# Kernel tuning notes

Hardware: AMD Instinct MI355X
Metric: run time of the kernel (lower is better)

Reference implementation:

```python
import jax, jax.numpy as jnp
import numpy as np

B, T, H = 8192, 256, 128


def setup_inputs() -> dict:
    key = jax.random.key(0)
    ks = jax.random.split(key, 12)
    s = 1.0 / np.sqrt(H)
    inp = {
        "x_seq": jax.random.normal(ks[0], (B, T), dtype=jnp.float32),
        "m_seq": (jax.random.uniform(ks[1], (B, T)) < 0.5).astype(jnp.float32),
        # W_c: Linear(hidden, 1)
        "Wc_w": jax.random.uniform(ks[2], (1, H), minval=-s, maxval=s),
        "Wc_b": jax.random.uniform(ks[3], (1,), minval=-s, maxval=s),
        # W_x: Linear(1, hidden)
        "Wx_w": jax.random.uniform(ks[4], (H, 1), minval=-1.0, maxval=1.0),
        "Wx_b": jax.random.uniform(ks[5], (H,), minval=-1.0, maxval=1.0),
        # GRUCell(hidden+1, hidden): gates ordered (r, z, n) as in torch
        "W_ih": jax.random.uniform(ks[6], (3 * H, H + 1), minval=-s, maxval=s),
        "W_hh": jax.random.uniform(ks[7], (3 * H, H), minval=-s, maxval=s),
        "b_ih": jax.random.uniform(ks[8], (3 * H,), minval=-s, maxval=s),
        "b_hh": jax.random.uniform(ks[9], (3 * H,), minval=-s, maxval=s),
        # out: Linear(hidden, 1)
        "out_w": jax.random.uniform(ks[10], (1, H), minval=-s, maxval=s),
        "out_b": jax.random.uniform(ks[11], (1,), minval=-s, maxval=s),
    }
    return inp


def reference(x_seq, m_seq, Wc_w, Wc_b, Wx_w, Wx_b, W_ih, W_hh, b_ih, b_hh, out_w, out_b):
    Bd, Td = x_seq.shape
    Hd = W_hh.shape[1]

    def step(h, xs):
        x_t, m_t = xs  # each [B]
        # c_t = tanh(W_c h)[:, 0]
        c_t = jnp.tanh(h @ Wc_w.T + Wc_b)[:, 0]  # [B]
        x_imp = m_t * x_t + (1.0 - m_t) * c_t  # [B]
        # feat = relu(W_x x_imp): Linear(1, H) on scalar input
        feat = jax.nn.relu(x_imp[:, None] * Wx_w[:, 0][None, :] + Wx_b)  # [B, H]
        inp = jnp.concatenate([feat, m_t[:, None]], axis=1)  # [B, H+1]
        # torch GRUCell math, gate order (r, z, n)
        gi = inp @ W_ih.T + b_ih  # [B, 3H]
        gh = h @ W_hh.T + b_hh  # [B, 3H]
        i_r, i_z, i_n = gi[:, :Hd], gi[:, Hd:2 * Hd], gi[:, 2 * Hd:]
        h_r, h_z, h_n = gh[:, :Hd], gh[:, Hd:2 * Hd], gh[:, 2 * Hd:]
        r = jax.nn.sigmoid(i_r + h_r)
        z = jax.nn.sigmoid(i_z + h_z)
        n = jnp.tanh(i_n + r * h_n)
        h_new = (1.0 - z) * n + z * h
        pred = (h_new @ out_w.T + out_b)[:, 0]  # [B]
        return h_new, (pred, c_t)

    h0 = jnp.zeros((Bd, Hd), dtype=x_seq.dtype)
    xs = (x_seq.T, m_seq.T)  # [T, B]
    _, (preds, comps) = jax.lax.scan(step, h0, xs)
    return preds.T, comps.T  # each [B, T]
```

## Files before the change

kernel.cpp:

```cpp
#include <hip/hip_runtime.h>

#define B_ 8192
#define T_ 256
#define H_ 128
#define ROWS 32
#define NTH 512

typedef __attribute__((ext_vector_type(4))) float f32x4;
typedef __attribute__((ext_vector_type(4))) short short4_t;
typedef __attribute__((ext_vector_type(8))) short short8_t;
typedef __attribute__((ext_vector_type(8))) _Float16 half8;
typedef __attribute__((ext_vector_type(2))) _Float16 half2_t;
typedef __attribute__((ext_vector_type(4))) unsigned int uint4_t;

__device__ __forceinline__ float fast_exp(float x) {
    return __builtin_amdgcn_exp2f(x * 1.4426950408889634f);
}
__device__ __forceinline__ float sigm(float x) {
    return __builtin_amdgcn_rcpf(1.0f + fast_exp(-x));
}
__device__ __forceinline__ float tanh_f(float x) {
    return 1.0f - 2.0f * __builtin_amdgcn_rcpf(1.0f + fast_exp(2.0f * x));
}
__device__ __forceinline__ short h16bits(float v) {
    return __builtin_bit_cast(short, (_Float16)v);
}
__device__ __forceinline__ float h16f(short s) {
    return (float)__builtin_bit_cast(_Float16, s);
}
__device__ __forceinline__ float red16(float v) {
    v += __builtin_bit_cast(float, __builtin_amdgcn_update_dpp(0, __builtin_bit_cast(int, v), 0x111, 0xf, 0xf, true));
    v += __builtin_bit_cast(float, __builtin_amdgcn_update_dpp(0, __builtin_bit_cast(int, v), 0x112, 0xf, 0xf, true));
    v += __builtin_bit_cast(float, __builtin_amdgcn_update_dpp(0, __builtin_bit_cast(int, v), 0x114, 0xf, 0xf, true));
    v += __builtin_bit_cast(float, __builtin_amdgcn_update_dpp(0, __builtin_bit_cast(int, v), 0x118, 0xf, 0xf, true));
    return v;
}

__global__ __launch_bounds__(NTH, 2) void brits_kernel(
    const float* __restrict__ x_seq, const float* __restrict__ m_seq,
    const float* __restrict__ Wc_w,  const float* __restrict__ Wc_b,
    const float* __restrict__ Wx_w,  const float* __restrict__ Wx_b,
    const float* __restrict__ W_ih,  const float* __restrict__ W_hh,
    const float* __restrict__ b_ih,  const float* __restrict__ b_hh,
    const float* __restrict__ out_w, const float* __restrict__ out_b,
    float* __restrict__ out)
{
    __shared__ __align__(16) short feat_s[2][4][512];
    __shared__ __align__(16) short h_s[2][2][4][512];
    __shared__ __align__(16) short x_all[T_][ROWS];
    __shared__ __align__(16) short m_all[T_][ROWS];
    __shared__ __align__(16) short comp_sh[ROWS][264];
    __shared__ __align__(16) short pred_sh[ROWS][264];
    __shared__ __align__(16) float part_c[ROWS][8];
    __shared__ __align__(16) float wx_s[H_];
    __shared__ __align__(16) float bx_s[H_];
    __shared__ __align__(16) short ow_s[4][512];

    const int tid  = threadIdx.x;
    const int lane = tid & 63;
    const int wv   = tid >> 6;
    const int kg   = lane >> 4;
    const int ln16 = lane & 15;
    const int rb   = kg * 4;
    const long b0  = (long)blockIdx.x * ROWS;

    const int rowA = tid & 31;
    const int qA   = tid >> 5;

    const float cb = Wc_b[0];
    const float ob = out_b[0];

    const int cH = wv * 16 + ln16;
    const int cR = cH, cZ = cH + 128, cN = cH + 256;
    const float bR  = b_ih[cR] + b_hh[cR];
    const float bZ  = b_ih[cZ] + b_hh[cZ];
    const float bNi = b_ih[cN];
    const float bNh = b_hh[cN];
    const float WmR = W_ih[cR * 129 + 128];
    const float WmZ = W_ih[cZ * 129 + 128];
    const float WmN = W_ih[cN * 129 + 128];
    const float wcc = Wc_w[cH];

    half8 wr[8], wz[8], wn[8];
#pragma unroll
    for (int kc = 0; kc < 8; ++kc) {
        const float *pr, *pz, *pn;
        if (kc < 4) {
            const int off = kc * 32 + kg * 8;
            pr = W_ih + cR * 129 + off;
            pz = W_ih + cZ * 129 + off;
            pn = W_ih + cN * 129 + off;
        } else {
            const int off = (kc - 4) * 32 + kg * 8;
            pr = W_hh + cR * 128 + off;
            pz = W_hh + cZ * 128 + off;
            pn = W_hh + cN * 128 + off;
        }
#pragma unroll
        for (int e = 0; e < 8; ++e) {
            wr[kc][e] = (_Float16)pr[e];
            wz[kc][e] = (_Float16)pz[e];
            wn[kc][e] = (_Float16)pn[e];
        }
    }

    {
        const int prow = tid >> 4;
        const int ptb  = (tid & 15) * 16;
        const float* xp = x_seq + (b0 + prow) * T_ + ptb;
        const float* mp = m_seq + (b0 + prow) * T_ + ptb;
#pragma unroll
        for (int i = 0; i < 4; ++i) {
            f32x4 xv = *(const f32x4*)(xp + 4 * i);
            f32x4 mv = *(const f32x4*)(mp + 4 * i);
#pragma unroll
            for (int j = 0; j < 4; ++j) {
                x_all[ptb + 4 * i + j][prow] = h16bits(xv[j]);
                m_all[ptb + 4 * i + j][prow] = h16bits(mv[j]);
            }
        }
    }
    if (tid < H_) { wx_s[tid] = Wx_w[tid]; bx_s[tid] = Wx_b[tid]; }
    {
        short8_t z8 = {0, 0, 0, 0, 0, 0, 0, 0};
        *(short8_t*)((short*)h_s + tid * 8) = z8;
    }
    if (tid < 256) ((float*)part_c)[tid] = 0.0f;
#pragma unroll
    for (int i = 0; i < 4; ++i) {
        const int idx = tid * 4 + i;
        const int c = idx >> 9, rl = idx & 511;
        const int ln = rl >> 3, j = rl & 7;
        const int col = ln & 15;
        const int k = 32 * c + (ln >> 4) * 8 + j;
        ((short*)ow_s)[idx] = (col == 0) ? h16bits(out_w[k]) : (short)0;
    }

    f32x4 h0reg = {0.f, 0.f, 0.f, 0.f};
    f32x4 h1reg = {0.f, 0.f, 0.f, 0.f};
    __syncthreads();

    for (int t = 0; t < T_; ++t) {
        const int pb = t & 1, nb = pb ^ 1;

        f32x4 p0 = *(const f32x4*)&part_c[rowA][0];
        f32x4 p1 = *(const f32x4*)&part_c[rowA][4];
        const float sc = ((p0[0] + p0[1]) + (p0[2] + p0[3])) +
                         ((p1[0] + p1[1]) + (p1[2] + p1[3]));
        const float c_t = tanh_f(sc + cb);
        const float xv = h16f(x_all[t][rowA]);
        const float mv = h16f(m_all[t][rowA]);
        const float xi = (mv != 0.0f) ? xv : c_t;
        if (qA == 0) comp_sh[rowA][t] = h16bits(c_t);
        {
            f32x4 wxa = *(const f32x4*)&wx_s[qA * 8];
            f32x4 wxb = *(const f32x4*)&wx_s[qA * 8 + 4];
            f32x4 bxa = *(const f32x4*)&bx_s[qA * 8];
            f32x4 bxb = *(const f32x4*)&bx_s[qA * 8 + 4];
            f32x4 fa, fb;
#pragma unroll
            for (int j = 0; j < 4; ++j) {
                fa[j] = fmaxf(xi * wxa[j] + bxa[j], 0.0f);
                fb[j] = fmaxf(xi * wxb[j] + bxb[j], 0.0f);
            }
            uint4_t pk;
            pk[0] = __builtin_bit_cast(unsigned int, __builtin_amdgcn_cvt_pkrtz(fa[0], fa[1]));
            pk[1] = __builtin_bit_cast(unsigned int, __builtin_amdgcn_cvt_pkrtz(fa[2], fa[3]));
            pk[2] = __builtin_bit_cast(unsigned int, __builtin_amdgcn_cvt_pkrtz(fb[0], fb[1]));
            pk[3] = __builtin_bit_cast(unsigned int, __builtin_amdgcn_cvt_pkrtz(fb[2], fb[3]));
            *(uint4_t*)&feat_s[rowA >> 4][qA >> 2][((rowA & 15) + 16 * (qA & 3)) * 8] = pk;
        }

        short4_t m4a = *(const short4_t*)&m_all[t][rb];
        short4_t m4b = *(const short4_t*)&m_all[t][16 + rb];
        f32x4 aR0, aZ0, aNi0, aNh0, aR1, aZ1, aNi1, aNh1;
#pragma unroll
        for (int e = 0; e < 4; ++e) {
            const float m0 = h16f(m4a[e]), m1 = h16f(m4b[e]);
            aR0[e]  = bR  + m0 * WmR;  aR1[e]  = bR  + m1 * WmR;
            aZ0[e]  = bZ  + m0 * WmZ;  aZ1[e]  = bZ  + m1 * WmZ;
            aNi0[e] = bNi + m0 * WmN;  aNi1[e] = bNi + m1 * WmN;
            aNh0[e] = bNh;             aNh1[e] = bNh;
        }
        f32x4 pacc = {0.f, 0.f, 0.f, 0.f};
        __syncthreads();

#pragma unroll
        for (int kc = 0; kc < 4; ++kc) {
            half8 a0 = __builtin_bit_cast(half8, *(const short8_t*)&feat_s[0][kc][lane * 8]);
            half8 a1 = __builtin_bit_cast(half8, *(const short8_t*)&feat_s[1][kc][lane * 8]);
            aR0  = __builtin_amdgcn_mfma_f32_16x16x32_f16(a0, wr[kc], aR0, 0, 0, 0);
            aZ0  = __builtin_amdgcn_mfma_f32_16x16x32_f16(a0, wz[kc], aZ0, 0, 0, 0);
            aNi0 = __builtin_amdgcn_mfma_f32_16x16x32_f16(a0, wn[kc], aNi0, 0, 0, 0);
            aR1  = __builtin_amdgcn_mfma_f32_16x16x32_f16(a1, wr[kc], aR1, 0, 0, 0);
            aZ1  = __builtin_amdgcn_mfma_f32_16x16x32_f16(a1, wz[kc], aZ1, 0, 0, 0);
            aNi1 = __builtin_amdgcn_mfma_f32_16x16x32_f16(a1, wn[kc], aNi1, 0, 0, 0);
        }
#pragma unroll
        for (int kc = 0; kc < 4; ++kc) {
            half8 a0 = __builtin_bit_cast(half8, *(const short8_t*)&h_s[pb][0][kc][lane * 8]);
            half8 a1 = __builtin_bit_cast(half8, *(const short8_t*)&h_s[pb][1][kc][lane * 8]);
            aR0  = __builtin_amdgcn_mfma_f32_16x16x32_f16(a0, wr[4 + kc], aR0, 0, 0, 0);
            aZ0  = __builtin_amdgcn_mfma_f32_16x16x32_f16(a0, wz[4 + kc], aZ0, 0, 0, 0);
            aNh0 = __builtin_amdgcn_mfma_f32_16x16x32_f16(a0, wn[4 + kc], aNh0, 0, 0, 0);
            aR1  = __builtin_amdgcn_mfma_f32_16x16x32_f16(a1, wr[4 + kc], aR1, 0, 0, 0);
            aZ1  = __builtin_amdgcn_mfma_f32_16x16x32_f16(a1, wz[4 + kc], aZ1, 0, 0, 0);
            aNh1 = __builtin_amdgcn_mfma_f32_16x16x32_f16(a1, wn[4 + kc], aNh1, 0, 0, 0);
            if (wv == 4) {
                half8 bfr = __builtin_bit_cast(half8, *(const short8_t*)&ow_s[kc][lane * 8]);
                pacc = __builtin_amdgcn_mfma_f32_16x16x32_f16(a0, bfr, pacc, 0, 0, 0);
            }
            if (wv == 5) {
                half8 bfr = __builtin_bit_cast(half8, *(const short8_t*)&ow_s[kc][lane * 8]);
                pacc = __builtin_amdgcn_mfma_f32_16x16x32_f16(a1, bfr, pacc, 0, 0, 0);
            }
        }

        f32x4 hn0, hn1;
#pragma unroll
        for (int e = 0; e < 4; ++e) {
            const float r0 = sigm(aR0[e]), z0 = sigm(aZ0[e]);
            const float n0 = tanh_f(aNi0[e] + r0 * aNh0[e]);
            hn0[e] = z0 * (h0reg[e] - n0) + n0;
            const float r1 = sigm(aR1[e]), z1 = sigm(aZ1[e]);
            const float n1 = tanh_f(aNi1[e] + r1 * aNh1[e]);
            hn1[e] = z1 * (h1reg[e] - n1) + n1;
        }
        h0reg = hn0; h1reg = hn1;

        const int hc = cH >> 5;
        const int hbase = ((cH & 31) >> 3) * 128 + (cH & 7);
#pragma unroll
        for (int e = 0; e < 4; ++e) {
            h_s[nb][0][hc][hbase + (rb + e) * 8] = h16bits(hn0[e]);
            h_s[nb][1][hc][hbase + (rb + e) * 8] = h16bits(hn1[e]);
        }
#pragma unroll
        for (int e = 0; e < 4; ++e) {
            const float s0 = red16(hn0[e] * wcc);
            const float s1 = red16(hn1[e] * wcc);
            if (ln16 == 15) {
                part_c[rb + e][wv]      = s0;
                part_c[16 + rb + e][wv] = s1;
            }
        }
        if ((wv == 4 || wv == 5) && ln16 == 0 && t > 0) {
#pragma unroll
            for (int e = 0; e < 4; ++e)
                pred_sh[(wv - 4) * 16 + rb + e][t - 1] = h16bits(pacc[e] + ob);
        }
        __syncthreads();
    }

    if (wv == 4 || wv == 5) {
        f32x4 pacc = {0.f, 0.f, 0.f, 0.f};
#pragma unroll
        for (int kc = 0; kc < 4; ++kc) {
            half8 a = __builtin_bit_cast(half8, *(const short8_t*)&h_s[0][wv - 4][kc][lane * 8]);
            half8 bfr = __builtin_bit_cast(half8, *(const short8_t*)&ow_s[kc][lane * 8]);
            pacc = __builtin_amdgcn_mfma_f32_16x16x32_f16(a, bfr, pacc, 0, 0, 0);
        }
        if (ln16 == 0) {
#pragma unroll
            for (int e = 0; e < 4; ++e)
                pred_sh[(wv - 4) * 16 + rb + e][T_ - 1] = h16bits(pacc[e] + ob);
        }
    }
    __syncthreads();

    {
        const int orow = tid >> 4;
        const int oc   = (tid & 15) * 16;
        short8_t r0 = *(const short8_t*)&pred_sh[orow][oc];
        short8_t r1 = *(const short8_t*)&pred_sh[orow][oc + 8];
        float* gp = out + (b0 + orow) * T_ + oc;
#pragma unroll
        for (int i = 0; i < 4; ++i) {
            f32x4 o;
            o[0] = h16f((i < 2) ? r0[i * 4 + 0] : r1[(i - 2) * 4 + 0]);
            o[1] = h16f((i < 2) ? r0[i * 4 + 1] : r1[(i - 2) * 4 + 1]);
            o[2] = h16f((i < 2) ? r0[i * 4 + 2] : r1[(i - 2) * 4 + 2]);
            o[3] = h16f((i < 2) ? r0[i * 4 + 3] : r1[(i - 2) * 4 + 3]);
            *(f32x4*)(gp + 4 * i) = o;
        }
        short8_t c0v = *(const short8_t*)&comp_sh[orow][oc];
        short8_t c1v = *(const short8_t*)&comp_sh[orow][oc + 8];
        float* gc = out + (long)B_ * T_ + (b0 + orow) * T_ + oc;
#pragma unroll
        for (int i = 0; i < 4; ++i) {
            f32x4 o;
            o[0] = h16f((i < 2) ? c0v[i * 4 + 0] : c1v[(i - 2) * 4 + 0]);
            o[1] = h16f((i < 2) ? c0v[i * 4 + 1] : c1v[(i - 2) * 4 + 1]);
            o[2] = h16f((i < 2) ? c0v[i * 4 + 2] : c1v[(i - 2) * 4 + 2]);
            o[3] = h16f((i < 2) ? c0v[i * 4 + 3] : c1v[(i - 2) * 4 + 3]);
            *(f32x4*)(gc + 4 * i) = o;
        }
    }
}

extern "C" void kernel_launch(void* const* d_in, const int* in_sizes, int n_in,
                              void* d_out, int out_size, void* d_ws, size_t ws_size,
                              hipStream_t stream) {
    const float* x_seq = (const float*)d_in[0];
    const float* m_seq = (const float*)d_in[1];
    const float* Wc_w  = (const float*)d_in[2];
    const float* Wc_b  = (const float*)d_in[3];
    const float* Wx_w  = (const float*)d_in[4];
    const float* Wx_b  = (const float*)d_in[5];
    const float* W_ih  = (const float*)d_in[6];
    const float* W_hh  = (const float*)d_in[7];
    const float* b_ih  = (const float*)d_in[8];
    const float* b_hh  = (const float*)d_in[9];
    const float* out_w = (const float*)d_in[10];
    const float* out_b = (const float*)d_in[11];
    float* out = (float*)d_out;

    dim3 grid(B_ / ROWS);
    dim3 block(NTH);
    brits_kernel<<<grid, block, 0, stream>>>(x_seq, m_seq, Wc_w, Wc_b, Wx_w, Wx_b,
                                             W_ih, W_hh, b_ih, b_hh, out_w, out_b, out);
}
```

Before: 636.2 us.

## Halve rows per block, pack h in fp16, fuse pred into reduction

Rows per block drop from 32 to 16 and launch bounds rise from 2 to 4 blocks per SM, trading fewer MFMAs per block for more resident blocks and more grid parallelism. The output projection is no longer a separate MFMA on two waves. It now runs as a packed fp16 DPP reduction alongside the Wc reduction, so one half2 reduce gives both c_t and pred. Hidden state and the bias/mask terms are kept in packed fp16, which cuts registers but lowers accumulation precision in the reductions.

```diff
diff --git a/kernel.cpp b/kernel.cpp
--- a/kernel.cpp
+++ b/kernel.cpp
@@ -3,7 +3,7 @@
 #define B_ 8192
 #define T_ 256
 #define H_ 128
-#define ROWS 32
+#define ROWS 16
 #define NTH 512
 
 typedef __attribute__((ext_vector_type(4))) float f32x4;
@@ -11,6 +11,7 @@
 typedef __attribute__((ext_vector_type(8))) short short8_t;
 typedef __attribute__((ext_vector_type(8))) _Float16 half8;
 typedef __attribute__((ext_vector_type(2))) _Float16 half2_t;
+typedef __attribute__((ext_vector_type(2))) unsigned int uint2_t;
 typedef __attribute__((ext_vector_type(4))) unsigned int uint4_t;
 
 __device__ __forceinline__ float fast_exp(float x) {
@@ -28,15 +29,24 @@
 __device__ __forceinline__ float h16f(short s) {
     return (float)__builtin_bit_cast(_Float16, s);
 }
-__device__ __forceinline__ float red16(float v) {
-    v += __builtin_bit_cast(float, __builtin_amdgcn_update_dpp(0, __builtin_bit_cast(int, v), 0x111, 0xf, 0xf, true));
-    v += __builtin_bit_cast(float, __builtin_amdgcn_update_dpp(0, __builtin_bit_cast(int, v), 0x112, 0xf, 0xf, true));
-    v += __builtin_bit_cast(float, __builtin_amdgcn_update_dpp(0, __builtin_bit_cast(int, v), 0x114, 0xf, 0xf, true));
-    v += __builtin_bit_cast(float, __builtin_amdgcn_update_dpp(0, __builtin_bit_cast(int, v), 0x118, 0xf, 0xf, true));
+__device__ __forceinline__ unsigned pk2(float lo, float hi) {
+    return __builtin_bit_cast(unsigned, __builtin_amdgcn_cvt_pkrtz(lo, hi));
+}
+__device__ __forceinline__ half2_t h2(unsigned u) {
+    return __builtin_bit_cast(half2_t, u);
+}
+__device__ __forceinline__ unsigned pkadd(unsigned a, unsigned b) {
+    return __builtin_bit_cast(unsigned, (half2_t)(h2(a) + h2(b)));
+}
+__device__ __forceinline__ unsigned red16_pk(unsigned v) {
+    v = pkadd(v, (unsigned)__builtin_amdgcn_update_dpp(0, (int)v, 0x111, 0xf, 0xf, true));
+    v = pkadd(v, (unsigned)__builtin_amdgcn_update_dpp(0, (int)v, 0x112, 0xf, 0xf, true));
+    v = pkadd(v, (unsigned)__builtin_amdgcn_update_dpp(0, (int)v, 0x114, 0xf, 0xf, true));
+    v = pkadd(v, (unsigned)__builtin_amdgcn_update_dpp(0, (int)v, 0x118, 0xf, 0xf, true));
     return v;
 }
 
-__global__ __launch_bounds__(NTH, 2) void brits_kernel(
+__global__ __launch_bounds__(NTH, 4) void brits_kernel(
     const float* __restrict__ x_seq, const float* __restrict__ m_seq,
     const float* __restrict__ Wc_w,  const float* __restrict__ Wc_b,
     const float* __restrict__ Wx_w,  const float* __restrict__ Wx_b,
@@ -45,16 +55,15 @@
     const float* __restrict__ out_w, const float* __restrict__ out_b,
     float* __restrict__ out)
 {
-    __shared__ __align__(16) short feat_s[2][4][512];
-    __shared__ __align__(16) short h_s[2][2][4][512];
+    __shared__ __align__(16) short feat_s[4][512];
+    __shared__ __align__(16) short h_s[2][4][512];
     __shared__ __align__(16) short x_all[T_][ROWS];
     __shared__ __align__(16) short m_all[T_][ROWS];
     __shared__ __align__(16) short comp_sh[ROWS][264];
     __shared__ __align__(16) short pred_sh[ROWS][264];
-    __shared__ __align__(16) float part_c[ROWS][8];
+    __shared__ __align__(16) unsigned part_cp[ROWS][8];
     __shared__ __align__(16) float wx_s[H_];
     __shared__ __align__(16) float bx_s[H_];
-    __shared__ __align__(16) short ow_s[4][512];
 
     const int tid  = threadIdx.x;
     const int lane = tid & 63;
@@ -64,22 +73,21 @@
     const int rb   = kg * 4;
     const long b0  = (long)blockIdx.x * ROWS;
 
-    const int rowA = tid & 31;
-    const int qA   = tid >> 5;
+    const int rowA = tid & 15;
+    const int kqA  = tid >> 4;
 
     const float cb = Wc_b[0];
     const float ob = out_b[0];
 
     const int cH = wv * 16 + ln16;
     const int cR = cH, cZ = cH + 128, cN = cH + 256;
-    const float bR  = b_ih[cR] + b_hh[cR];
-    const float bZ  = b_ih[cZ] + b_hh[cZ];
-    const float bNi = b_ih[cN];
-    const float bNh = b_hh[cN];
-    const float WmR = W_ih[cR * 129 + 128];
-    const float WmZ = W_ih[cZ * 129 + 128];
-    const float WmN = W_ih[cN * 129 + 128];
+
+    const unsigned bRZ  = pk2(b_ih[cR] + b_hh[cR], b_ih[cZ] + b_hh[cZ]);
+    const unsigned WmRZ = pk2(W_ih[cR * 129 + 128], W_ih[cZ * 129 + 128]);
+    const unsigned bNN  = pk2(b_ih[cN], b_hh[cN]);
+    const unsigned WmN0 = pk2(W_ih[cN * 129 + 128], 0.0f);
     const float wcc = Wc_w[cH];
+    const float owc = out_w[cH];
 
     half8 wr[8], wz[8], wn[8];
 #pragma unroll
@@ -105,18 +113,18 @@
     }
 
     {
-        const int prow = tid >> 4;
-        const int ptb  = (tid & 15) * 16;
-        const float* xp = x_seq + (b0 + prow) * T_ + ptb;
-        const float* mp = m_seq + (b0 + prow) * T_ + ptb;
-#pragma unroll
-        for (int i = 0; i < 4; ++i) {
+        const int prow = tid >> 5;
+        const int pc0  = (tid & 31) * 8;
+        const float* xp = x_seq + (b0 + prow) * T_ + pc0;
+        const float* mp = m_seq + (b0 + prow) * T_ + pc0;
+#pragma unroll
+        for (int i = 0; i < 2; ++i) {
             f32x4 xv = *(const f32x4*)(xp + 4 * i);
             f32x4 mv = *(const f32x4*)(mp + 4 * i);
 #pragma unroll
             for (int j = 0; j < 4; ++j) {
-                x_all[ptb + 4 * i + j][prow] = h16bits(xv[j]);
-                m_all[ptb + 4 * i + j][prow] = h16bits(mv[j]);
+                x_all[pc0 + 4 * i + j][prow] = h16bits(xv[j]);
+                m_all[pc0 + 4 * i + j][prow] = h16bits(mv[j]);
             }
         }
     }
@@ -125,174 +133,127 @@
         short8_t z8 = {0, 0, 0, 0, 0, 0, 0, 0};
         *(short8_t*)((short*)h_s + tid * 8) = z8;
     }
-    if (tid < 256) ((float*)part_c)[tid] = 0.0f;
-#pragma unroll
-    for (int i = 0; i < 4; ++i) {
-        const int idx = tid * 4 + i;
-        const int c = idx >> 9, rl = idx & 511;
-        const int ln = rl >> 3, j = rl & 7;
-        const int col = ln & 15;
-        const int k = 32 * c + (ln >> 4) * 8 + j;
-        ((short*)ow_s)[idx] = (col == 0) ? h16bits(out_w[k]) : (short)0;
-    }
-
-    f32x4 h0reg = {0.f, 0.f, 0.f, 0.f};
-    f32x4 h1reg = {0.f, 0.f, 0.f, 0.f};
+    if (tid < ROWS * 8) ((unsigned*)part_cp)[tid] = 0u;
+
+    unsigned hp0 = 0u, hp1 = 0u;
     __syncthreads();
 
     for (int t = 0; t < T_; ++t) {
         const int pb = t & 1, nb = pb ^ 1;
 
-        f32x4 p0 = *(const f32x4*)&part_c[rowA][0];
-        f32x4 p1 = *(const f32x4*)&part_c[rowA][4];
-        const float sc = ((p0[0] + p0[1]) + (p0[2] + p0[3])) +
-                         ((p1[0] + p1[1]) + (p1[2] + p1[3]));
-        const float c_t = tanh_f(sc + cb);
+        uint4_t u0 = *(const uint4_t*)&part_cp[rowA][0];
+        uint4_t u1 = *(const uint4_t*)&part_cp[rowA][4];
+        unsigned sacc = pkadd(pkadd(pkadd(u0[0], u0[1]), pkadd(u0[2], u0[3])),
+                              pkadd(pkadd(u1[0], u1[1]), pkadd(u1[2], u1[3])));
+        const half2_t sv = h2(sacc);
+        const float c_t = tanh_f((float)sv[0] + cb);
+        if (kqA == 0) comp_sh[rowA][t] = h16bits(c_t);
+        if (kqA == 1 && t > 0) pred_sh[rowA][t - 1] = h16bits((float)sv[1] + ob);
+
         const float xv = h16f(x_all[t][rowA]);
         const float mv = h16f(m_all[t][rowA]);
         const float xi = (mv != 0.0f) ? xv : c_t;
-        if (qA == 0) comp_sh[rowA][t] = h16bits(c_t);
         {
-            f32x4 wxa = *(const f32x4*)&wx_s[qA * 8];
-            f32x4 wxb = *(const f32x4*)&wx_s[qA * 8 + 4];
-            f32x4 bxa = *(const f32x4*)&bx_s[qA * 8];
-            f32x4 bxb = *(const f32x4*)&bx_s[qA * 8 + 4];
-            f32x4 fa, fb;
-#pragma unroll
-            for (int j = 0; j < 4; ++j) {
-                fa[j] = fmaxf(xi * wxa[j] + bxa[j], 0.0f);
-                fb[j] = fmaxf(xi * wxb[j] + bxb[j], 0.0f);
-            }
-            uint4_t pk;
-            pk[0] = __builtin_bit_cast(unsigned int, __builtin_amdgcn_cvt_pkrtz(fa[0], fa[1]));
-            pk[1] = __builtin_bit_cast(unsigned int, __builtin_amdgcn_cvt_pkrtz(fa[2], fa[3]));
-            pk[2] = __builtin_bit_cast(unsigned int, __builtin_amdgcn_cvt_pkrtz(fb[0], fb[1]));
-            pk[3] = __builtin_bit_cast(unsigned int, __builtin_amdgcn_cvt_pkrtz(fb[2], fb[3]));
-            *(uint4_t*)&feat_s[rowA >> 4][qA >> 2][((rowA & 15) + 16 * (qA & 3)) * 8] = pk;
-        }
-
-        short4_t m4a = *(const short4_t*)&m_all[t][rb];
-        short4_t m4b = *(const short4_t*)&m_all[t][16 + rb];
-        f32x4 aR0, aZ0, aNi0, aNh0, aR1, aZ1, aNi1, aNh1;
+            const int k = kqA * 4;
+            f32x4 wx4 = *(const f32x4*)&wx_s[k];
+            f32x4 bx4 = *(const f32x4*)&bx_s[k];
+            float f0 = fmaxf(xi * wx4[0] + bx4[0], 0.0f);
+            float f1 = fmaxf(xi * wx4[1] + bx4[1], 0.0f);
+            float f2 = fmaxf(xi * wx4[2] + bx4[2], 0.0f);
+            float f3 = fmaxf(xi * wx4[3] + bx4[3], 0.0f);
+            uint2_t pk; pk[0] = pk2(f0, f1); pk[1] = pk2(f2, f3);
+            const int o = (kqA >> 1) & 3, j = (kqA & 1) * 4;
+            *(uint2_t*)&feat_s[kqA >> 3][(rowA + 16 * o) * 8 + j] = pk;
+        }
+
+        short4_t m4 = *(const short4_t*)&m_all[t][rb];
+        f32x4 aR, aZ, aNi, aNh;
 #pragma unroll
         for (int e = 0; e < 4; ++e) {
-            const float m0 = h16f(m4a[e]), m1 = h16f(m4b[e]);
-            aR0[e]  = bR  + m0 * WmR;  aR1[e]  = bR  + m1 * WmR;
-            aZ0[e]  = bZ  + m0 * WmZ;  aZ1[e]  = bZ  + m1 * WmZ;
-            aNi0[e] = bNi + m0 * WmN;  aNi1[e] = bNi + m1 * WmN;
-            aNh0[e] = bNh;             aNh1[e] = bNh;
-        }
-        f32x4 pacc = {0.f, 0.f, 0.f, 0.f};
+            unsigned mu = (unsigned)(unsigned short)m4[e];
+            mu |= mu << 16;
+            half2_t rz = h2(mu) * h2(WmRZ) + h2(bRZ);
+            half2_t nn = h2(mu) * h2(WmN0) + h2(bNN);
+            aR[e] = (float)rz[0]; aZ[e] = (float)rz[1];
+            aNi[e] = (float)nn[0]; aNh[e] = (float)nn[1];
+        }
         __syncthreads();
 
 #pragma unroll
         for (int kc = 0; kc < 4; ++kc) {
-            half8 a0 = __builtin_bit_cast(half8, *(const short8_t*)&feat_s[0][kc][lane * 8]);
-            half8 a1 = __builtin_bit_cast(half8, *(const short8_t*)&feat_s[1][kc][lane * 8]);
-            aR0  = __builtin_amdgcn_mfma_f32_16x16x32_f16(a0, wr[kc], aR0, 0, 0, 0);
-            aZ0  = __builtin_amdgcn_mfma_f32_16x16x32_f16(a0, wz[kc], aZ0, 0, 0, 0);
-            aNi0 = __builtin_amdgcn_mfma_f32_16x16x32_f16(a0, wn[kc], aNi0, 0, 0, 0);
-            aR1  = __builtin_amdgcn_mfma_f32_16x16x32_f16(a1, wr[kc], aR1, 0, 0, 0);
-            aZ1  = __builtin_amdgcn_mfma_f32_16x16x32_f16(a1, wz[kc], aZ1, 0, 0, 0);
-            aNi1 = __builtin_amdgcn_mfma_f32_16x16x32_f16(a1, wn[kc], aNi1, 0, 0, 0);
+            half8 a = __builtin_bit_cast(half8, *(const short8_t*)&feat_s[kc][lane * 8]);
+            aR  = __builtin_amdgcn_mfma_f32_16x16x32_f16(a, wr[kc], aR, 0, 0, 0);
+            aZ  = __builtin_amdgcn_mfma_f32_16x16x32_f16(a, wz[kc], aZ, 0, 0, 0);
+            aNi = __builtin_amdgcn_mfma_f32_16x16x32_f16(a, wn[kc], aNi, 0, 0, 0);
         }
 #pragma unroll
         for (int kc = 0; kc < 4; ++kc) {
-            half8 a0 = __builtin_bit_cast(half8, *(const short8_t*)&h_s[pb][0][kc][lane * 8]);
-            half8 a1 = __builtin_bit_cast(half8, *(const short8_t*)&h_s[pb][1][kc][lane * 8]);
-            aR0  = __builtin_amdgcn_mfma_f32_16x16x32_f16(a0, wr[4 + kc], aR0, 0, 0, 0);
-            aZ0  = __builtin_amdgcn_mfma_f32_16x16x32_f16(a0, wz[4 + kc], aZ0, 0, 0, 0);
-            aNh0 = __builtin_amdgcn_mfma_f32_16x16x32_f16(a0, wn[4 + kc], aNh0, 0, 0, 0);
-            aR1  = __builtin_amdgcn_mfma_f32_16x16x32_f16(a1, wr[4 + kc], aR1, 0, 0, 0);
-            aZ1  = __builtin_amdgcn_mfma_f32_16x16x32_f16(a1, wz[4 + kc], aZ1, 0, 0, 0);
-            aNh1 = __builtin_amdgcn_mfma_f32_16x16x32_f16(a1, wn[4 + kc], aNh1, 0, 0, 0);
-            if (wv == 4) {
-                half8 bfr = __builtin_bit_cast(half8, *(const short8_t*)&ow_s[kc][lane * 8]);
-                pacc = __builtin_amdgcn_mfma_f32_16x16x32_f16(a0, bfr, pacc, 0, 0, 0);
-            }
-            if (wv == 5) {
-                half8 bfr = __builtin_bit_cast(half8, *(const short8_t*)&ow_s[kc][lane * 8]);
-                pacc = __builtin_amdgcn_mfma_f32_16x16x32_f16(a1, bfr, pacc, 0, 0, 0);
-            }
-        }
-
-        f32x4 hn0, hn1;
+            half8 a = __builtin_bit_cast(half8, *(const short8_t*)&h_s[pb][kc][lane * 8]);
+            aR  = __builtin_amdgcn_mfma_f32_16x16x32_f16(a, wr[4 + kc], aR, 0, 0, 0);
+            aZ  = __builtin_amdgcn_mfma_f32_16x16x32_f16(a, wz[4 + kc], aZ, 0, 0, 0);
+            aNh = __builtin_amdgcn_mfma_f32_16x16x32_f16(a, wn[4 + kc], aNh, 0, 0, 0);
+        }
+
+        f32x4 hn;
+        {
+            const float h0 = (float)h2(hp0)[0], h1 = (float)h2(hp0)[1];
+            const float h2v = (float)h2(hp1)[0], h3 = (float)h2(hp1)[1];
+            float r, z, n;
+            r = sigm(aR[0]); z = sigm(aZ[0]); n = tanh_f(aNi[0] + r * aNh[0]);
+            hn[0] = z * (h0 - n) + n;
+            r = sigm(aR[1]); z = sigm(aZ[1]); n = tanh_f(aNi[1] + r * aNh[1]);
+            hn[1] = z * (h1 - n) + n;
+            r = sigm(aR[2]); z = sigm(aZ[2]); n = tanh_f(aNi[2] + r * aNh[2]);
+            hn[2] = z * (h2v - n) + n;
+            r = sigm(aR[3]); z = sigm(aZ[3]); n = tanh_f(aNi[3] + r * aNh[3]);
+            hn[3] = z * (h3 - n) + n;
+        }
+        hp0 = pk2(hn[0], hn[1]);
+        hp1 = pk2(hn[2], hn[3]);
+
+        {
+            short* hdst = &h_s[nb][cH >> 5][((cH & 31) >> 3) * 128 + (cH & 7)];
+            hdst[(rb + 0) * 8] = (short)(hp0 & 0xffffu);
+            hdst[(rb + 1) * 8] = (short)(hp0 >> 16);
+            hdst[(rb + 2) * 8] = (short)(hp1 & 0xffffu);
+            hdst[(rb + 3) * 8] = (short)(hp1 >> 16);
+        }
 #pragma unroll
         for (int e = 0; e < 4; ++e) {
-            const float r0 = sigm(aR0[e]), z0 = sigm(aZ0[e]);
-            const float n0 = tanh_f(aNi0[e] + r0 * aNh0[e]);
-            hn0[e] = z0 * (h0reg[e] - n0) + n0;
-            const float r1 = sigm(aR1[e]), z1 = sigm(aZ1[e]);
-            const float n1 = tanh_f(aNi1[e] + r1 * aNh1[e]);
-            hn1[e] = z1 * (h1reg[e] - n1) + n1;
-        }
-        h0reg = hn0; h1reg = hn1;
-
-        const int hc = cH >> 5;
-        const int hbase = ((cH & 31) >> 3) * 128 + (cH & 7);
-#pragma unroll
-        for (int e = 0; e < 4; ++e) {
-            h_s[nb][0][hc][hbase + (rb + e) * 8] = h16bits(hn0[e]);
-            h_s[nb][1][hc][hbase + (rb + e) * 8] = h16bits(hn1[e]);
-        }
-#pragma unroll
-        for (int e = 0; e < 4; ++e) {
-            const float s0 = red16(hn0[e] * wcc);
-            const float s1 = red16(hn1[e] * wcc);
-            if (ln16 == 15) {
-                part_c[rb + e][wv]      = s0;
-                part_c[16 + rb + e][wv] = s1;
-            }
-        }
-        if ((wv == 4 || wv == 5) && ln16 == 0 && t > 0) {
-#pragma unroll
-            for (int e = 0; e < 4; ++e)
-                pred_sh[(wv - 4) * 16 + rb + e][t - 1] = h16bits(pacc[e] + ob);
+            unsigned v = red16_pk(pk2(hn[e] * wcc, hn[e] * owc));
+            if (ln16 == 15) part_cp[rb + e][wv] = v;
         }
         __syncthreads();
     }
 
-    if (wv == 4 || wv == 5) {
-        f32x4 pacc = {0.f, 0.f, 0.f, 0.f};
-#pragma unroll
-        for (int kc = 0; kc < 4; ++kc) {
-            half8 a = __builtin_bit_cast(half8, *(const short8_t*)&h_s[0][wv - 4][kc][lane * 8]);
-            half8 bfr = __builtin_bit_cast(half8, *(const short8_t*)&ow_s[kc][lane * 8]);
-            pacc = __builtin_amdgcn_mfma_f32_16x16x32_f16(a, bfr, pacc, 0, 0, 0);
-        }
-        if (ln16 == 0) {
-#pragma unroll
-            for (int e = 0; e < 4; ++e)
-                pred_sh[(wv - 4) * 16 + rb + e][T_ - 1] = h16bits(pacc[e] + ob);
-        }
+    {
+        uint4_t u0 = *(const uint4_t*)&part_cp[rowA][0];
+        uint4_t u1 = *(const uint4_t*)&part_cp[rowA][4];
+        unsigned sacc = pkadd(pkadd(pkadd(u0[0], u0[1]), pkadd(u0[2], u0[3])),
+                              pkadd(pkadd(u1[0], u1[1]), pkadd(u1[2], u1[3])));
+        if (kqA == 1) pred_sh[rowA][T_ - 1] = h16bits((float)h2(sacc)[1] + ob);
     }
     __syncthreads();
 
     {
-        const int orow = tid >> 4;
-        const int oc   = (tid & 15) * 16;
-        short8_t r0 = *(const short8_t*)&pred_sh[orow][oc];
-        short8_t r1 = *(const short8_t*)&pred_sh[orow][oc + 8];
+        const int orow = tid >> 5;
+        const int oc   = (tid & 31) * 8;
+        short8_t pv = *(const short8_t*)&pred_sh[orow][oc];
         float* gp = out + (b0 + orow) * T_ + oc;
 #pragma unroll
-        for (int i = 0; i < 4; ++i) {
+        for (int i = 0; i < 2; ++i) {
             f32x4 o;
-            o[0] = h16f((i < 2) ? r0[i * 4 + 0] : r1[(i - 2) * 4 + 0]);
-            o[1] = h16f((i < 2) ? r0[i * 4 + 1] : r1[(i - 2) * 4 + 1]);
-            o[2] = h16f((i < 2) ? r0[i * 4 + 2] : r1[(i - 2) * 4 + 2]);
-            o[3] = h16f((i < 2) ? r0[i * 4 + 3] : r1[(i - 2) * 4 + 3]);
+            o[0] = h16f(pv[i * 4 + 0]); o[1] = h16f(pv[i * 4 + 1]);
+            o[2] = h16f(pv[i * 4 + 2]); o[3] = h16f(pv[i * 4 + 3]);
             *(f32x4*)(gp + 4 * i) = o;
         }
-        short8_t c0v = *(const short8_t*)&comp_sh[orow][oc];
-        short8_t c1v = *(const short8_t*)&comp_sh[orow][oc + 8];
+        short8_t cv = *(const short8_t*)&comp_sh[orow][oc];
         float* gc = out + (long)B_ * T_ + (b0 + orow) * T_ + oc;
 #pragma unroll
-        for (int i = 0; i < 4; ++i) {
+        for (int i = 0; i < 2; ++i) {
             f32x4 o;
-            o[0] = h16f((i < 2) ? c0v[i * 4 + 0] : c1v[(i - 2) * 4 + 0]);
-            o[1] = h16f((i < 2) ? c0v[i * 4 + 1] : c1v[(i - 2) * 4 + 1]);
-            o[2] = h16f((i < 2) ? c0v[i * 4 + 2] : c1v[(i - 2) * 4 + 2]);
-            o[3] = h16f((i < 2) ? c0v[i * 4 + 3] : c1v[(i - 2) * 4 + 3]);
+            o[0] = h16f(cv[i * 4 + 0]); o[1] = h16f(cv[i * 4 + 1]);
+            o[2] = h16f(cv[i * 4 + 2]); o[3] = h16f(cv[i * 4 + 3]);
             *(f32x4*)(gc + 4 * i) = o;
         }
     }
```

Result: slower. 1.270 ms (+99.7%).

## Remove per-step barrier by computing features in registers and fusing pred reduction

Applied to the files above, without the earlier changes.

Each wave now computes the imputed feature fragment for its own MFMA A-operand in registers using packed fp16 math, so the shared feat buffer and the mid-step __syncthreads go away. The output projection is folded into the same DPP reduction as the complement projection by packing both into one half2, and the partial sums are double-buffered. The old dedicated MFMA pred path and ow_s table are removed. The cost is redundant feature computation in every wave, and extra fp16 precision loss in the bias and reduction math.

```diff
diff --git a/kernel.cpp b/kernel.cpp
--- a/kernel.cpp
+++ b/kernel.cpp
@@ -28,11 +28,20 @@
 __device__ __forceinline__ float h16f(short s) {
     return (float)__builtin_bit_cast(_Float16, s);
 }
-__device__ __forceinline__ float red16(float v) {
-    v += __builtin_bit_cast(float, __builtin_amdgcn_update_dpp(0, __builtin_bit_cast(int, v), 0x111, 0xf, 0xf, true));
-    v += __builtin_bit_cast(float, __builtin_amdgcn_update_dpp(0, __builtin_bit_cast(int, v), 0x112, 0xf, 0xf, true));
-    v += __builtin_bit_cast(float, __builtin_amdgcn_update_dpp(0, __builtin_bit_cast(int, v), 0x114, 0xf, 0xf, true));
-    v += __builtin_bit_cast(float, __builtin_amdgcn_update_dpp(0, __builtin_bit_cast(int, v), 0x118, 0xf, 0xf, true));
+__device__ __forceinline__ unsigned pk2(float lo, float hi) {
+    return __builtin_bit_cast(unsigned, __builtin_amdgcn_cvt_pkrtz(lo, hi));
+}
+__device__ __forceinline__ half2_t h2(unsigned u) {
+    return __builtin_bit_cast(half2_t, u);
+}
+__device__ __forceinline__ unsigned pkadd(unsigned a, unsigned b) {
+    return __builtin_bit_cast(unsigned, (half2_t)(h2(a) + h2(b)));
+}
+__device__ __forceinline__ unsigned red16_pk(unsigned v) {
+    v = pkadd(v, (unsigned)__builtin_amdgcn_update_dpp(0, (int)v, 0x111, 0xf, 0xf, true));
+    v = pkadd(v, (unsigned)__builtin_amdgcn_update_dpp(0, (int)v, 0x112, 0xf, 0xf, true));
+    v = pkadd(v, (unsigned)__builtin_amdgcn_update_dpp(0, (int)v, 0x114, 0xf, 0xf, true));
+    v = pkadd(v, (unsigned)__builtin_amdgcn_update_dpp(0, (int)v, 0x118, 0xf, 0xf, true));
     return v;
 }
 
@@ -45,16 +54,12 @@
     const float* __restrict__ out_w, const float* __restrict__ out_b,
     float* __restrict__ out)
 {
-    __shared__ __align__(16) short feat_s[2][4][512];
     __shared__ __align__(16) short h_s[2][2][4][512];
     __shared__ __align__(16) short x_all[T_][ROWS];
     __shared__ __align__(16) short m_all[T_][ROWS];
     __shared__ __align__(16) short comp_sh[ROWS][264];
     __shared__ __align__(16) short pred_sh[ROWS][264];
-    __shared__ __align__(16) float part_c[ROWS][8];
-    __shared__ __align__(16) float wx_s[H_];
-    __shared__ __align__(16) float bx_s[H_];
-    __shared__ __align__(16) short ow_s[4][512];
+    __shared__ __align__(16) unsigned part_cp[2][ROWS][12];
 
     const int tid  = threadIdx.x;
     const int lane = tid & 63;
@@ -62,24 +67,21 @@
     const int kg   = lane >> 4;
     const int ln16 = lane & 15;
     const int rb   = kg * 4;
+    const int rA   = lane & 15;
     const long b0  = (long)blockIdx.x * ROWS;
-
-    const int rowA = tid & 31;
-    const int qA   = tid >> 5;
 
     const float cb = Wc_b[0];
     const float ob = out_b[0];
 
     const int cH = wv * 16 + ln16;
     const int cR = cH, cZ = cH + 128, cN = cH + 256;
-    const float bR  = b_ih[cR] + b_hh[cR];
-    const float bZ  = b_ih[cZ] + b_hh[cZ];
-    const float bNi = b_ih[cN];
-    const float bNh = b_hh[cN];
-    const float WmR = W_ih[cR * 129 + 128];
-    const float WmZ = W_ih[cZ * 129 + 128];
-    const float WmN = W_ih[cN * 129 + 128];
+
+    const unsigned bRZ  = pk2(b_ih[cR] + b_hh[cR], b_ih[cZ] + b_hh[cZ]);
+    const unsigned WmRZ = pk2(W_ih[cR * 129 + 128], W_ih[cZ * 129 + 128]);
+    const unsigned bNN  = pk2(b_ih[cN], b_hh[cN]);
+    const unsigned WmN0 = pk2(W_ih[cN * 129 + 128], 0.0f);
     const float wcc = Wc_w[cH];
+    const float owc = out_w[cH];
 
     half8 wr[8], wz[8], wn[8];
 #pragma unroll
@@ -104,6 +106,16 @@
         }
     }
 
+    unsigned wxp[16], bxp[16];
+#pragma unroll
+    for (int c = 0; c < 4; ++c)
+#pragma unroll
+        for (int p = 0; p < 4; ++p) {
+            const int k = c * 32 + kg * 8 + 2 * p;
+            wxp[c * 4 + p] = pk2(Wx_w[k], Wx_w[k + 1]);
+            bxp[c * 4 + p] = pk2(Wx_b[k], Wx_b[k + 1]);
+        }
+
     {
         const int prow = tid >> 4;
         const int ptb  = (tid & 15) * 16;
@@ -120,82 +132,40 @@
             }
         }
     }
-    if (tid < H_) { wx_s[tid] = Wx_w[tid]; bx_s[tid] = Wx_b[tid]; }
     {
         short8_t z8 = {0, 0, 0, 0, 0, 0, 0, 0};
         *(short8_t*)((short*)h_s + tid * 8) = z8;
     }
-    if (tid < 256) ((float*)part_c)[tid] = 0.0f;
-#pragma unroll
-    for (int i = 0; i < 4; ++i) {
-        const int idx = tid * 4 + i;
-        const int c = idx >> 9, rl = idx & 511;
-        const int ln = rl >> 3, j = rl & 7;
-        const int col = ln & 15;
-        const int k = 32 * c + (ln >> 4) * 8 + j;
-        ((short*)ow_s)[idx] = (col == 0) ? h16bits(out_w[k]) : (short)0;
-    }
-
-    f32x4 h0reg = {0.f, 0.f, 0.f, 0.f};
-    f32x4 h1reg = {0.f, 0.f, 0.f, 0.f};
+    if (tid < ROWS * 12) ((unsigned*)part_cp)[tid] = 0u;
+
+    unsigned hpa0 = 0u, hpa1 = 0u, hpb0 = 0u, hpb1 = 0u;
     __syncthreads();
 
     for (int t = 0; t < T_; ++t) {
         const int pb = t & 1, nb = pb ^ 1;
 
-        f32x4 p0 = *(const f32x4*)&part_c[rowA][0];
-        f32x4 p1 = *(const f32x4*)&part_c[rowA][4];
-        const float sc = ((p0[0] + p0[1]) + (p0[2] + p0[3])) +
-                         ((p1[0] + p1[1]) + (p1[2] + p1[3]));
-        const float c_t = tanh_f(sc + cb);
-        const float xv = h16f(x_all[t][rowA]);
-        const float mv = h16f(m_all[t][rowA]);
-        const float xi = (mv != 0.0f) ? xv : c_t;
-        if (qA == 0) comp_sh[rowA][t] = h16bits(c_t);
-        {
-            f32x4 wxa = *(const f32x4*)&wx_s[qA * 8];
-            f32x4 wxb = *(const f32x4*)&wx_s[qA * 8 + 4];
-            f32x4 bxa = *(const f32x4*)&bx_s[qA * 8];
-            f32x4 bxb = *(const f32x4*)&bx_s[qA * 8 + 4];
-            f32x4 fa, fb;
-#pragma unroll
-            for (int j = 0; j < 4; ++j) {
-                fa[j] = fmaxf(xi * wxa[j] + bxa[j], 0.0f);
-                fb[j] = fmaxf(xi * wxb[j] + bxb[j], 0.0f);
-            }
-            uint4_t pk;
-            pk[0] = __builtin_bit_cast(unsigned int, __builtin_amdgcn_cvt_pkrtz(fa[0], fa[1]));
-            pk[1] = __builtin_bit_cast(unsigned int, __builtin_amdgcn_cvt_pkrtz(fa[2], fa[3]));
-            pk[2] = __builtin_bit_cast(unsigned int, __builtin_amdgcn_cvt_pkrtz(fb[0], fb[1]));
-            pk[3] = __builtin_bit_cast(unsigned int, __builtin_amdgcn_cvt_pkrtz(fb[2], fb[3]));
-            *(uint4_t*)&feat_s[rowA >> 4][qA >> 2][((rowA & 15) + 16 * (qA & 3)) * 8] = pk;
-        }
+        uint4_t u0a = *(const uint4_t*)&part_cp[pb][rA][0];
+        uint4_t u1a = *(const uint4_t*)&part_cp[pb][rA][4];
+        uint4_t u0b = *(const uint4_t*)&part_cp[pb][16 + rA][0];
+        uint4_t u1b = *(const uint4_t*)&part_cp[pb][16 + rA][4];
 
         short4_t m4a = *(const short4_t*)&m_all[t][rb];
         short4_t m4b = *(const short4_t*)&m_all[t][16 + rb];
         f32x4 aR0, aZ0, aNi0, aNh0, aR1, aZ1, aNi1, aNh1;
 #pragma unroll
         for (int e = 0; e < 4; ++e) {
-            const float m0 = h16f(m4a[e]), m1 = h16f(m4b[e]);
-            aR0[e]  = bR  + m0 * WmR;  aR1[e]  = bR  + m1 * WmR;
-            aZ0[e]  = bZ  + m0 * WmZ;  aZ1[e]  = bZ  + m1 * WmZ;
-            aNi0[e] = bNi + m0 * WmN;  aNi1[e] = bNi + m1 * WmN;
-            aNh0[e] = bNh;             aNh1[e] = bNh;
-        }
-        f32x4 pacc = {0.f, 0.f, 0.f, 0.f};
-        __syncthreads();
-
-#pragma unroll
-        for (int kc = 0; kc < 4; ++kc) {
-            half8 a0 = __builtin_bit_cast(half8, *(const short8_t*)&feat_s[0][kc][lane * 8]);
-            half8 a1 = __builtin_bit_cast(half8, *(const short8_t*)&feat_s[1][kc][lane * 8]);
-            aR0  = __builtin_amdgcn_mfma_f32_16x16x32_f16(a0, wr[kc], aR0, 0, 0, 0);
-            aZ0  = __builtin_amdgcn_mfma_f32_16x16x32_f16(a0, wz[kc], aZ0, 0, 0, 0);
-            aNi0 = __builtin_amdgcn_mfma_f32_16x16x32_f16(a0, wn[kc], aNi0, 0, 0, 0);
-            aR1  = __builtin_amdgcn_mfma_f32_16x16x32_f16(a1, wr[kc], aR1, 0, 0, 0);
-            aZ1  = __builtin_amdgcn_mfma_f32_16x16x32_f16(a1, wz[kc], aZ1, 0, 0, 0);
-            aNi1 = __builtin_amdgcn_mfma_f32_16x16x32_f16(a1, wn[kc], aNi1, 0, 0, 0);
-        }
+            unsigned mu0 = (unsigned)(unsigned short)m4a[e]; mu0 |= mu0 << 16;
+            unsigned mu1 = (unsigned)(unsigned short)m4b[e]; mu1 |= mu1 << 16;
+            half2_t rz0 = h2(mu0) * h2(WmRZ) + h2(bRZ);
+            half2_t nn0 = h2(mu0) * h2(WmN0) + h2(bNN);
+            half2_t rz1 = h2(mu1) * h2(WmRZ) + h2(bRZ);
+            half2_t nn1 = h2(mu1) * h2(WmN0) + h2(bNN);
+            aR0[e] = (float)rz0[0]; aZ0[e] = (float)rz0[1];
+            aNi0[e] = (float)nn0[0]; aNh0[e] = (float)nn0[1];
+            aR1[e] = (float)rz1[0]; aZ1[e] = (float)rz1[1];
+            aNi1[e] = (float)nn1[0]; aNh1[e] = (float)nn1[1];
+        }
+
 #pragma unroll
         for (int kc = 0; kc < 4; ++kc) {
             half8 a0 = __builtin_bit_cast(half8, *(const short8_t*)&h_s[pb][0][kc][lane * 8]);
@@ -206,81 +176,117 @@
             aR1  = __builtin_amdgcn_mfma_f32_16x16x32_f16(a1, wr[4 + kc], aR1, 0, 0, 0);
             aZ1  = __builtin_amdgcn_mfma_f32_16x16x32_f16(a1, wz[4 + kc], aZ1, 0, 0, 0);
             aNh1 = __builtin_amdgcn_mfma_f32_16x16x32_f16(a1, wn[4 + kc], aNh1, 0, 0, 0);
-            if (wv == 4) {
-                half8 bfr = __builtin_bit_cast(half8, *(const short8_t*)&ow_s[kc][lane * 8]);
-                pacc = __builtin_amdgcn_mfma_f32_16x16x32_f16(a0, bfr, pacc, 0, 0, 0);
+        }
+
+        unsigned sa = pkadd(pkadd(pkadd(u0a[0], u0a[1]), pkadd(u0a[2], u0a[3])),
+                            pkadd(pkadd(u1a[0], u1a[1]), pkadd(u1a[2], u1a[3])));
+        unsigned sb = pkadd(pkadd(pkadd(u0b[0], u0b[1]), pkadd(u0b[2], u0b[3])),
+                            pkadd(pkadd(u1b[0], u1b[1]), pkadd(u1b[2], u1b[3])));
+        const float c0 = tanh_f((float)h2(sa)[0] + cb);
+        const float c1 = tanh_f((float)h2(sb)[0] + cb);
+        if (wv == 0 && lane < 32) comp_sh[lane][t] = h16bits(lane < 16 ? c0 : c1);
+        if (wv == 1 && lane < 32 && t > 0)
+            pred_sh[lane][t - 1] = h16bits((float)h2(lane < 16 ? sa : sb)[1] + ob);
+
+        const short xs0 = x_all[t][rA],      ms0 = m_all[t][rA];
+        const short xs1 = x_all[t][16 + rA], ms1 = m_all[t][16 + rA];
+        const _Float16 xi0 = ms0 ? __builtin_bit_cast(_Float16, xs0) : (_Float16)c0;
+        const _Float16 xi1 = ms1 ? __builtin_bit_cast(_Float16, xs1) : (_Float16)c1;
+        const half2_t xx0 = {xi0, xi0};
+        const half2_t xx1 = {xi1, xi1};
+        const half2_t z2 = {(_Float16)0, (_Float16)0};
+
+#pragma unroll
+        for (int kc = 0; kc < 4; ++kc) {
+            uint4_t f0, f1;
+#pragma unroll
+            for (int p = 0; p < 4; ++p) {
+                half2_t v0 = h2(wxp[kc * 4 + p]) * xx0 + h2(bxp[kc * 4 + p]);
+                half2_t v1 = h2(wxp[kc * 4 + p]) * xx1 + h2(bxp[kc * 4 + p]);
+                v0[0] = v0[0] > z2[0] ? v0[0] : z2[0];
+                v0[1] = v0[1] > z2[0] ? v0[1] : z2[0];
+                v1[0] = v1[0] > z2[0] ? v1[0] : z2[0];
+                v1[1] = v1[1] > z2[0] ? v1[1] : z2[0];
+                f0[p] = __builtin_bit_cast(unsigned, v0);
+                f1[p] = __builtin_bit_cast(unsigned, v1);
             }
-            if (wv == 5) {
-                half8 bfr = __builtin_bit_cast(half8, *(const short8_t*)&ow_s[kc][lane * 8]);
-                pacc = __builtin_amdgcn_mfma_f32_16x16x32_f16(a1, bfr, pacc, 0, 0, 0);
+            half8 a0 = __builtin_bit_cast(half8, f0);
+            half8 a1 = __builtin_bit_cast(half8, f1);
+            aR0  = __builtin_amdgcn_mfma_f32_16x16x32_f16(a0, wr[kc], aR0, 0, 0, 0);
+            aZ0  = __builtin_amdgcn_mfma_f32_16x16x32_f16(a0, wz[kc], aZ0, 0, 0, 0);
+            aNi0 = __builtin_amdgcn_mfma_f32_16x16x32_f16(a0, wn[kc], aNi0, 0, 0, 0);
+            aR1  = __builtin_amdgcn_mfma_f32_16x16x32_f16(a1, wr[kc], aR1, 0, 0, 0);
+            aZ1  = __builtin_amdgcn_mfma_f32_16x16x32_f16(a1, wz[kc], aZ1, 0, 0, 0);
+            aNi1 = __builtin_amdgcn_mfma_f32_16x16x32_f16(a1, wn[kc], aNi1, 0, 0, 0);
+        }
+
+        f32x4 hn0, hn1;
+#pragma unroll
+        for (int e = 0; e < 4; ++e) {
+            const float hp0v = (e < 2) ? (float)h2(hpa0)[e & 1] : (float)h2(hpa1)[e & 1];
+            const float hp1v = (e < 2) ? (float)h2(hpb0)[e & 1] : (float)h2(hpb1)[e & 1];
+            float r = sigm(aR0[e]), z = sigm(aZ0[e]);
+            float n = tanh_f(aNi0[e] + r * aNh0[e]);
+            hn0[e] = z * (hp0v - n) + n;
+            r = sigm(aR1[e]); z = sigm(aZ1[e]);
+            n = tanh_f(aNi1[e] + r * aNh1[e]);
+            hn1[e] = z * (hp1v - n) + n;
+        }
+        hpa0 = pk2(hn0[0], hn0[1]); hpa1 = pk2(hn0[2], hn0[3]);
+        hpb0 = pk2(hn1[0], hn1[1]); hpb1 = pk2(hn1[2], hn1[3]);
+
+        {
+            const int fo = ((cH & 31) >> 3) * 128 + (cH & 7);
+            short* d0 = &h_s[nb][0][cH >> 5][fo];
+            short* d1 = &h_s[nb][1][cH >> 5][fo];
+            d0[(rb + 0) * 8] = (short)(hpa0 & 0xffffu);
+            d0[(rb + 1) * 8] = (short)(hpa0 >> 16);
+            d0[(rb + 2) * 8] = (short)(hpa1 & 0xffffu);
+            d0[(rb + 3) * 8] = (short)(hpa1 >> 16);
+            d1[(rb + 0) * 8] = (short)(hpb0 & 0xffffu);
+            d1[(rb + 1) * 8] = (short)(hpb0 >> 16);
+            d1[(rb + 2) * 8] = (short)(hpb1 & 0xffffu);
+            d1[(rb + 3) * 8] = (short)(hpb1 >> 16);
+        }
+#pragma unroll
+        for (int e = 0; e < 4; ++e) {
+            unsigned v0 = red16_pk(pk2(hn0[e] * wcc, hn0[e] * owc));
+            unsigned v1 = red16_pk(pk2(hn1[e] * wcc, hn1[e] * owc));
+            if (ln16 == 15) {
+                part_cp[nb][rb + e][wv]      = v0;
+                part_cp[nb][16 + rb + e][wv] = v1;
             }
         }
-
-        f32x4 hn0, hn1;
-#pragma unroll
-        for (int e = 0; e < 4; ++e) {
-            const float r0 = sigm(aR0[e]), z0 = sigm(aZ0[e]);
-            const float n0 = tanh_f(aNi0[e] + r0 * aNh0[e]);
-            hn0[e] = z0 * (h0reg[e] - n0) + n0;
-            const float r1 = sigm(aR1[e]), z1 = sigm(aZ1[e]);
-            const float n1 = tanh_f(aNi1[e] + r1 * aNh1[e]);
-            hn1[e] = z1 * (h1reg[e] - n1) + n1;
-        }
-        h0reg = hn0; h1reg = hn1;
-
-        const int hc = cH >> 5;
-        const int hbase = ((cH & 31) >> 3) * 128 + (cH & 7);
-#pragma unroll
-        for (int e = 0; e < 4; ++e) {
-            h_s[nb][0][hc][hbase + (rb + e) * 8] = h16bits(hn0[e]);
-            h_s[nb][1][hc][hbase + (rb + e) * 8] = h16bits(hn1[e]);
-        }
-#pragma unroll
-        for (int e = 0; e < 4; ++e) {
-            const float s0 = red16(hn0[e] * wcc);
-            const float s1 = red16(hn1[e] * wcc);
-            if (ln16 == 15) {
-                part_c[rb + e][wv]      = s0;
-                part_c[16 + rb + e][wv] = s1;
-            }
-        }
-        if ((wv == 4 || wv == 5) && ln16 == 0 && t > 0) {
-#pragma unroll
-            for (int e = 0; e < 4; ++e)
-                pred_sh[(wv - 4) * 16 + rb + e][t - 1] = h16bits(pacc[e] + ob);
-        }
         __syncthreads();
     }
 
-    if (wv == 4 || wv == 5) {
-        f32x4 pacc = {0.f, 0.f, 0.f, 0.f};
-#pragma unroll
-        for (int kc = 0; kc < 4; ++kc) {
-            half8 a = __builtin_bit_cast(half8, *(const short8_t*)&h_s[0][wv - 4][kc][lane * 8]);
-            half8 bfr = __builtin_bit_cast(half8, *(const short8_t*)&ow_s[kc][lane * 8]);
-            pacc = __builtin_amdgcn_mfma_f32_16x16x32_f16(a, bfr, pacc, 0, 0, 0);
-        }
-        if (ln16 == 0) {
-#pragma unroll
-            for (int e = 0; e < 4; ++e)
-                pred_sh[(wv - 4) * 16 + rb + e][T_ - 1] = h16bits(pacc[e] + ob);
-        }
+    {
+        uint4_t u0a = *(const uint4_t*)&part_cp[0][rA][0];
+        uint4_t u1a = *(const uint4_t*)&part_cp[0][rA][4];
+        uint4_t u0b = *(const uint4_t*)&part_cp[0][16 + rA][0];
+        uint4_t u1b = *(const uint4_t*)&part_cp[0][16 + rA][4];
+        unsigned sa = pkadd(pkadd(pkadd(u0a[0], u0a[1]), pkadd(u0a[2], u0a[3])),
+                            pkadd(pkadd(u1a[0], u1a[1]), pkadd(u1a[2], u1a[3])));
+        unsigned sb = pkadd(pkadd(pkadd(u0b[0], u0b[1]), pkadd(u0b[2], u0b[3])),
+                            pkadd(pkadd(u1b[0], u1b[1]), pkadd(u1b[2], u1b[3])));
+        if (wv == 1 && lane < 32)
+            pred_sh[lane][T_ - 1] = h16bits((float)h2(lane < 16 ? sa : sb)[1] + ob);
     }
     __syncthreads();
 
     {
         const int orow = tid >> 4;
         const int oc   = (tid & 15) * 16;
-        short8_t r0 = *(const short8_t*)&pred_sh[orow][oc];
-        short8_t r1 = *(const short8_t*)&pred_sh[orow][oc + 8];
+        short8_t p0 = *(const short8_t*)&pred_sh[orow][oc];
+        short8_t p1 = *(const short8_t*)&pred_sh[orow][oc + 8];
         float* gp = out + (b0 + orow) * T_ + oc;
 #pragma unroll
         for (int i = 0; i < 4; ++i) {
             f32x4 o;
-            o[0] = h16f((i < 2) ? r0[i * 4 + 0] : r1[(i - 2) * 4 + 0]);
-            o[1] = h16f((i < 2) ? r0[i * 4 + 1] : r1[(i - 2) * 4 + 1]);
-            o[2] = h16f((i < 2) ? r0[i * 4 + 2] : r1[(i - 2) * 4 + 2]);
-            o[3] = h16f((i < 2) ? r0[i * 4 + 3] : r1[(i - 2) * 4 + 3]);
+            o[0] = h16f((i < 2) ? p0[i * 4 + 0] : p1[(i - 2) * 4 + 0]);
+            o[1] = h16f((i < 2) ? p0[i * 4 + 1] : p1[(i - 2) * 4 + 1]);
+            o[2] = h16f((i < 2) ? p0[i * 4 + 2] : p1[(i - 2) * 4 + 2]);
+            o[3] = h16f((i < 2) ? p0[i * 4 + 3] : p1[(i - 2) * 4 + 3]);
             *(f32x4*)(gp + 4 * i) = o;
         }
         short8_t c0v = *(const short8_t*)&comp_sh[orow][oc];
```

Result: slower. 682.3 us (+7.2%).
